# Kernel tuning notes

Hardware: AMD Instinct MI355X
Metric: run time of the kernel (lower is better)

The kernel has to match this reference:

```python
import jax, jax.numpy as jnp
import numpy as np

# GPT-2 decoder (mlm=False path of the Keras GPT module), no past/KV-cache,
# no explicit mask -> causal mask, dropout disabled (training=False).
N_HEAD = 12
NINF = -10000.0  # Attention.ninf
EPS = 1e-6


def layer_norm(x, g, b):
    m = jnp.mean(x, axis=-1, keepdims=True)
    v = jnp.mean(jnp.square(x - m), axis=-1, keepdims=True)
    return (x - m) / jnp.sqrt(v + EPS) * g + b


def gelu(x):
    # 0.5*x*(1+erf(x/sqrt(2))) as in gelu_activating
    return 0.5 * x * (1.0 + jax.lax.erf(x * np.float32(1.0 / np.sqrt(2.0))))


def setup_inputs() -> dict:
    key = jax.random.key(0)
    B, S, D, L, V, CTX = 4, 512, 768, 12, 50257, 1024
    F = 4 * D
    ks = jax.random.split(key, 10)
    init = lambda k, shape: (jax.random.normal(k, shape, jnp.float32) * 0.02)
    return {
        "x": jax.random.randint(ks[0], (B, S), 0, V),
        "emb": init(ks[1], (V, D)),        # wte (tied output projection)
        "posemb": init(ks[2], (CTX, D)),   # wpe
        "ln1_g": jnp.ones((L, D)), "ln1_b": jnp.zeros((L, D)),
        "wqkv": init(ks[3], (L, D, 3 * D)), "bqkv": jnp.zeros((L, 3 * D)),
        "wo": init(ks[4], (L, D, D)), "bo": jnp.zeros((L, D)),
        "ln2_g": jnp.ones((L, D)), "ln2_b": jnp.zeros((L, D)),
        "wfc": init(ks[5], (L, D, F)), "bfc": jnp.zeros((L, F)),
        "wproj": init(ks[6], (L, F, D)), "bproj": jnp.zeros((L, D)),
        "lnf_g": jnp.ones((D,)), "lnf_b": jnp.zeros((D,)),
    }


def reference(x, emb, posemb, ln1_g, ln1_b, wqkv, bqkv, wo, bo,
              ln2_g, ln2_b, wfc, bfc, wproj, bproj, lnf_g, lnf_b):
    B, S = x.shape
    L, D, _ = wqkv.shape
    H = N_HEAD
    hd = D // H
    scale = np.float32(1.0 / np.sqrt(hd))

    # Embedding (mlm=False): token + positional, no layernorm
    h = emb[x] + posemb[:S]  # [B,S,D]

    # causal mask: positions j > i get NINF (m1 = range(q)[:,None] < range(k)-k+q)
    mask = (jnp.arange(S)[:, None] < jnp.arange(S)[None, :]).astype(jnp.float32) * NINF

    for i in range(L):
        # pre-norm attention
        qkv = layer_norm(h, ln1_g[i], ln1_b[i]) @ wqkv[i] + bqkv[i]  # [B,S,3D]
        q, k, v = jnp.split(qkv, 3, axis=-1)
        q = q.reshape(B, S, H, hd).transpose(0, 2, 1, 3)  # [B,H,S,hd]
        k = k.reshape(B, S, H, hd).transpose(0, 2, 1, 3)
        v = v.reshape(B, S, H, hd).transpose(0, 2, 1, 3)
        scores = jnp.einsum('bhqd,bhkd->bhqk', q, k) * scale + mask
        a = jax.nn.softmax(scores, axis=-1)  # [B,H,S,S]
        o = jnp.einsum('bhqk,bhkd->bhqd', a, v)
        o = o.transpose(0, 2, 1, 3).reshape(B, S, D)
        h = h + (o @ wo[i] + bo[i])  # residual
        # pre-norm MLP
        m = layer_norm(h, ln2_g[i], ln2_b[i])
        h = h + (gelu(m @ wfc[i] + bfc[i]) @ wproj[i] + bproj[i])

    hidden = layer_norm(h, lnf_g, lnf_b)          # model/lnorm_f
    logits = hidden @ emb.T                        # tied embedding projection
    probs = jax.nn.softmax(logits, axis=-1)        # softmax=True
    return (probs, hidden)
```

## Files before the change

kernel.cpp:

```cpp
#include <hip/hip_runtime.h>
#include <hip/hip_bf16.h>

typedef __bf16 bf16_t;
typedef bf16_t bf16x8 __attribute__((ext_vector_type(8)));
typedef float  f32x4  __attribute__((ext_vector_type(4)));

__device__ __forceinline__ void gload16(const void* g, void* l) {
    __builtin_amdgcn_global_load_lds(
        (const __attribute__((address_space(1))) unsigned int*)g,
        (__attribute__((address_space(3))) unsigned int*)l, 16, 0, 0);
}

__device__ __forceinline__ void drain_and_barrier() {
    __builtin_amdgcn_sched_barrier(0);
    asm volatile("s_waitcnt vmcnt(0)" ::: "memory");
    __builtin_amdgcn_s_barrier();
    __builtin_amdgcn_sched_barrier(0);
}

__global__ void embed_kernel(const int* __restrict__ x,
                             const float* __restrict__ emb,
                             const float* __restrict__ pos,
                             float* __restrict__ h,
                             int S, int D, int total)
{
    int i = blockIdx.x * blockDim.x + threadIdx.x;
    if (i >= total) return;
    int d  = i % D;
    int bs = i / D;
    int s  = bs % S;
    h[i] = emb[(long long)x[bs] * D + d] + pos[(long long)s * D + d];
}

__global__ void convert_bf16(const float* __restrict__ in, bf16_t* __restrict__ out, int n4)
{
    int i = blockIdx.x * blockDim.x + threadIdx.x;
    for (; i < n4; i += gridDim.x * blockDim.x) {
        float4 v = ((const float4*)in)[i];
        bf16_t* o = out + (size_t)i * 4;
        o[0] = (bf16_t)v.x; o[1] = (bf16_t)v.y; o[2] = (bf16_t)v.z; o[3] = (bf16_t)v.w;
    }
}

__global__ __launch_bounds__(256) void transpose_to_bf16(
    const float* __restrict__ in, bf16_t* __restrict__ out, int K, int N)
{
    const float* ip = in  + (size_t)blockIdx.z * K * N;
    bf16_t*      op = out + (size_t)blockIdx.z * K * N;
    __shared__ float t[32][33];
    const int n0 = blockIdx.x * 32, k0 = blockIdx.y * 32;
    const int tx = threadIdx.x, ty = threadIdx.y;
#pragma unroll
    for (int u = 0; u < 4; ++u)
        t[ty + u * 8][tx] = ip[(size_t)(k0 + ty + u * 8) * N + (n0 + tx)];
    __syncthreads();
#pragma unroll
    for (int u = 0; u < 4; ++u)
        op[(size_t)(n0 + ty + u * 8) * K + (k0 + tx)] = (bf16_t)t[tx][ty + u * 8];
}

__global__ __launch_bounds__(256) void transpose_v(
    const bf16_t* __restrict__ qkv, bf16_t* __restrict__ vT)
{
    constexpr int S = 512, TD = 2304, D = 768, H = 12;
    const int z = blockIdx.y, bb = z / H, hh = z - bb * H;
    const int k0 = blockIdx.x * 64;
    const bf16_t* src = qkv + (size_t)(bb * S + k0) * TD + 2 * D + hh * 64;
    bf16_t* dst = vT + (size_t)z * 64 * S + k0;
    __shared__ bf16_t sm[64][68];
    const int c = threadIdx.x & 63, rq = threadIdx.x >> 6;
#pragma unroll
    for (int u = 0; u < 16; ++u) {
        const int r = u * 4 + rq;
        sm[r][c] = src[(size_t)r * TD + c];
    }
    __syncthreads();
#pragma unroll
    for (int u = 0; u < 16; ++u) {
        const int d = u * 4 + rq;
        dst[(size_t)d * S + c] = sm[c][d];
    }
}

__global__ __launch_bounds__(256) void layernorm_dual(
    const float* __restrict__ X, const float* __restrict__ g,
    const float* __restrict__ b, bf16_t* __restrict__ Yb,
    float* __restrict__ Yf, int D)
{
    const int row = blockIdx.x;
    const float* xr = X + (long long)row * D;
    const int tid = threadIdx.x;

    float vals[3];
    float s = 0.0f;
#pragma unroll
    for (int u = 0; u < 3; ++u) { vals[u] = xr[tid + u * 256]; s += vals[u]; }

    __shared__ float red[256];
    red[tid] = s;
    __syncthreads();
    for (int off = 128; off > 0; off >>= 1) {
        if (tid < off) red[tid] += red[tid + off];
        __syncthreads();
    }
    const float mean = red[0] / (float)D;
    __syncthreads();

    float vs = 0.0f;
#pragma unroll
    for (int u = 0; u < 3; ++u) { float d = vals[u] - mean; vs += d * d; }
    red[tid] = vs;
    __syncthreads();
    for (int off = 128; off > 0; off >>= 1) {
        if (tid < off) red[tid] += red[tid + off];
        __syncthreads();
    }
    const float var  = red[0] / (float)D;
    const float rstd = rsqrtf(var + 1e-6f);

#pragma unroll
    for (int u = 0; u < 3; ++u) {
        const int c = tid + u * 256;
        const float y = (vals[u] - mean) * rstd * g[c] + b[c];
        Yb[(long long)row * D + c] = (bf16_t)y;
        if (Yf) Yf[(long long)row * D + c] = y;
    }
}

__global__ __launch_bounds__(256) void flash_attn(
    const bf16_t* __restrict__ qkv, const bf16_t* __restrict__ vT,
    bf16_t* __restrict__ o)
{
    constexpr int S = 512, TD = 2304, D = 768, H = 12;
    const int qt = blockIdx.x;
    const int z  = blockIdx.y;
    const int bb = z / H, hh = z - bb * H;
    const int tid = threadIdx.x, lane = tid & 63, w = tid >> 6;
    const int fr = lane & 15, g = lane >> 4, sub = g * 8;

    __shared__ bf16_t kS[2][4096];
    __shared__ bf16_t vS[2][4096];
    __shared__ bf16_t pS[4][32 * 72];

    bf16x8 qf[2][2];
    const bf16_t* qbase = qkv + (size_t)(bb * S + qt * 128 + w * 32) * TD + hh * 64;
#pragma unroll
    for (int m = 0; m < 2; ++m)
#pragma unroll
        for (int ks = 0; ks < 2; ++ks) {
            bf16x8 v = *(const bf16x8*)&qbase[(size_t)(m * 16 + fr) * TD + ks * 32 + sub];
#pragma unroll
            for (int j = 0; j < 8; ++j) v[j] = v[j] * (bf16_t)0.125f;
            qf[m][ks] = v;
        }

    f32x4 oacc[2][4];
    float mrun[2][4], lrun[2][4];
#pragma unroll
    for (int m = 0; m < 2; ++m)
#pragma unroll
        for (int r = 0; r < 4; ++r) { mrun[m][r] = -3.0e38f; lrun[m][r] = 0.0f; }
#pragma unroll
    for (int m = 0; m < 2; ++m)
#pragma unroll
        for (int n = 0; n < 4; ++n)
            oacc[m][n] = (f32x4){0.f, 0.f, 0.f, 0.f};

    int qr[2][4];
#pragma unroll
    for (int m = 0; m < 2; ++m)
#pragma unroll
        for (int r = 0; r < 4; ++r)
            qr[m][r] = qt * 128 + w * 32 + m * 16 + g * 4 + r;

    const int srow8  = lane >> 3;
    const int schunk = (lane & 7) ^ (srow8 & 7);

    const bf16_t* kGbase = qkv + (size_t)(bb * S) * TD + D + hh * 64;
    const bf16_t* vGbase = vT + (size_t)z * 64 * S;
    const int nkv = 2 * qt + 2;

#define STAGE_KV(buf, t)                                                        \
    {                                                                           \
        _Pragma("unroll")                                                       \
        for (int it = 0; it < 2; ++it) {                                        \
            const int row = it * 32 + w * 8 + srow8;                            \
            gload16(kGbase + (size_t)((t) * 64 + row) * TD + schunk * 8,        \
                    &kS[buf][it * 2048 + w * 512]);                             \
            gload16(vGbase + (size_t)row * S + (t) * 64 + schunk * 8,           \
                    &vS[buf][it * 2048 + w * 512]);                             \
        }                                                                       \
    }

    STAGE_KV(0, 0);
    drain_and_barrier();

    int cur = 0;
    for (int t = 0; t < nkv; ++t) {
        if (t + 1 < nkv) STAGE_KV(cur ^ 1, t + 1);

        f32x4 sacc[2][4];
#pragma unroll
        for (int m = 0; m < 2; ++m)
#pragma unroll
            for (int n = 0; n < 4; ++n)
                sacc[m][n] = (f32x4){0.f, 0.f, 0.f, 0.f};
#pragma unroll
        for (int ks = 0; ks < 2; ++ks) {
            bf16x8 bK[4];
#pragma unroll
            for (int n = 0; n < 4; ++n) {
                const int rw = n * 16 + fr;
                const int c  = ks * 4 + g;
                bK[n] = *(const bf16x8*)&kS[cur][rw * 64 + ((c ^ (rw & 7)) << 3)];
            }
#pragma unroll
            for (int m = 0; m < 2; ++m)
#pragma unroll
                for (int n = 0; n < 4; ++n)
                    sacc[m][n] = __builtin_amdgcn_mfma_f32_16x16x32_bf16(
                        qf[m][ks], bK[n], sacc[m][n], 0, 0, 0);
        }

        if (t >= 2 * qt) {
#pragma unroll
            for (int m = 0; m < 2; ++m)
#pragma unroll
                for (int n = 0; n < 4; ++n) {
                    const int key = t * 64 + n * 16 + fr;
#pragma unroll
                    for (int r = 0; r < 4; ++r)
                        if (key > qr[m][r]) sacc[m][n][r] = -3.0e38f;
                }
        }

        float sf[2][4], rs[2][4];
#pragma unroll
        for (int m = 0; m < 2; ++m)
#pragma unroll
            for (int r = 0; r < 4; ++r) {
                float v = fmaxf(fmaxf(sacc[m][0][r], sacc[m][1][r]),
                                fmaxf(sacc[m][2][r], sacc[m][3][r]));
#pragma unroll
                for (int off = 1; off < 16; off <<= 1)
                    v = fmaxf(v, __shfl_xor(v, off));
                const float mn = fmaxf(mrun[m][r], v);
                sf[m][r] = __expf(mrun[m][r] - mn);
                mrun[m][r] = mn;
                lrun[m][r] *= sf[m][r];
            }
#pragma unroll
        for (int m = 0; m < 2; ++m)
#pragma unroll
            for (int n = 0; n < 4; ++n)
#pragma unroll
                for (int r = 0; r < 4; ++r)
                    oacc[m][n][r] *= sf[m][r];
#pragma unroll
        for (int m = 0; m < 2; ++m)
#pragma unroll
            for (int r = 0; r < 4; ++r) rs[m][r] = 0.0f;
#pragma unroll
        for (int m = 0; m < 2; ++m)
#pragma unroll
            for (int n = 0; n < 4; ++n)
#pragma unroll
                for (int r = 0; r < 4; ++r) {
                    const float p = __expf(sacc[m][n][r] - mrun[m][r]);
                    sacc[m][n][r] = p;
                    rs[m][r] += p;
                }
#pragma unroll
        for (int m = 0; m < 2; ++m)
#pragma unroll
            for (int r = 0; r < 4; ++r) {
                float v = rs[m][r];
#pragma unroll
                for (int off = 1; off < 16; off <<= 1) v += __shfl_xor(v, off);
                lrun[m][r] += v;
            }

        bf16_t* pw = pS[w];
#pragma unroll
        for (int m = 0; m < 2; ++m)
#pragma unroll
            for (int n = 0; n < 4; ++n)
#pragma unroll
                for (int r = 0; r < 4; ++r)
                    pw[(m * 16 + g * 4 + r) * 72 + n * 16 + fr] = (bf16_t)sacc[m][n][r];

#pragma unroll
        for (int ks = 0; ks < 2; ++ks) {
            bf16x8 pa[2], vb[4];
#pragma unroll
            for (int m = 0; m < 2; ++m)
                pa[m] = *(const bf16x8*)&pw[(m * 16 + fr) * 72 + ks * 32 + sub];
#pragma unroll
            for (int n = 0; n < 4; ++n) {
                const int rw = n * 16 + fr;
                const int c  = ks * 4 + g;
                vb[n] = *(const bf16x8*)&vS[cur][rw * 64 + ((c ^ (rw & 7)) << 3)];
            }
#pragma unroll
            for (int m = 0; m < 2; ++m)
#pragma unroll
                for (int n = 0; n < 4; ++n)
                    oacc[m][n] = __builtin_amdgcn_mfma_f32_16x16x32_bf16(
                        pa[m], vb[n], oacc[m][n], 0, 0, 0);
        }
        drain_and_barrier();
        cur ^= 1;
    }
#undef STAGE_KV

    bf16_t* obase = o + (size_t)(bb * S + qt * 128 + w * 32) * D + hh * 64;
#pragma unroll
    for (int m = 0; m < 2; ++m)
#pragma unroll
        for (int r = 0; r < 4; ++r) {
            const float inv = 1.0f / lrun[m][r];
#pragma unroll
            for (int n = 0; n < 4; ++n)
                obase[(size_t)(m * 16 + g * 4 + r) * D + n * 16 + fr] =
                    (bf16_t)(oacc[m][n][r] * inv);
        }
}

__global__ __launch_bounds__(256) void softmax_vocab(
    const bf16_t* __restrict__ logits, float* __restrict__ probs, int V, int Vp)
{
    const int tid = threadIdx.x;
    const bf16_t* lr = logits + (size_t)blockIdx.x * Vp;
    float* pr = probs + (size_t)blockIdx.x * V;
    const int n8 = V >> 3;

    float m = -3.0e38f, s = 0.0f;
    for (int c8 = tid; c8 < n8; c8 += 256) {
        const bf16x8 v = *(const bf16x8*)(lr + (size_t)c8 * 8);
        float f[8], lm = -3.0e38f;
#pragma unroll
        for (int j = 0; j < 8; ++j) { f[j] = (float)v[j]; lm = fmaxf(lm, f[j]); }
        if (lm > m) { s *= __expf(m - lm); m = lm; }
#pragma unroll
        for (int j = 0; j < 8; ++j) s += __expf(f[j] - m);
    }
    for (int c = n8 * 8 + tid; c < V; c += 256) {
        const float f = (float)lr[c];
        if (f > m) { s *= __expf(m - f); m = f; }
        s += __expf(f - m);
    }

    __shared__ float mS[256], sS[256];
    mS[tid] = m; sS[tid] = s;
    __syncthreads();
    for (int off = 128; off > 0; off >>= 1) {
        if (tid < off) {
            const float m1 = mS[tid], m2 = mS[tid + off];
            const float M_ = fmaxf(m1, m2);
            sS[tid] = sS[tid] * __expf(m1 - M_) + sS[tid + off] * __expf(m2 - M_);
            mS[tid] = M_;
        }
        __syncthreads();
    }
    const float M_  = mS[0];
    const float inv = 1.0f / sS[0];

    for (int c8 = tid; c8 < n8; c8 += 256) {
        const bf16x8 v = *(const bf16x8*)(lr + (size_t)c8 * 8);
#pragma unroll
        for (int j = 0; j < 8; ++j)
            pr[(size_t)c8 * 8 + j] = __expf((float)v[j] - M_) * inv;
    }
    for (int c = n8 * 8 + tid; c < V; c += 256)
        pr[c] = __expf((float)lr[c] - M_) * inv;
}

template<bool ADD, bool GELU_, bool OUTBF, bool DB, bool HALFN>
__device__ __forceinline__ void gemm_body(
    const bf16_t* __restrict__ A, const bf16_t* __restrict__ Bw,
    const float* __restrict__ bias, void* __restrict__ Cv,
    int M, int N, int K, int lda, int ldb, int ldc)
{
    constexpr int BN  = HALFN ? 64 : 128;
    constexpr int BUF = HALFN ? 12288 : 16384;
    __shared__ bf16_t lds[(DB ? 2 : 1) * BUF];

    const int tid  = threadIdx.x;
    const int lane = tid & 63;
    const int w    = tid >> 6;
    const int row0 = blockIdx.x * 128;
    const int col0 = blockIdx.y * BN;

    const int row8 = lane >> 3;
    const int sch  = (lane & 7) ^ row8;
    const int fr   = lane & 15;
    const int g    = lane >> 4;

    const int aRowB = row0 + w * 32;
    const int bRowB = HALFN ? (col0 + w * 16) : (col0 + w * 32);

    constexpr int MR = HALFN ? 2 : 4;
    const int wr = HALFN ? w : (w >> 1);
    const int wc = HALFN ? 0 : (w & 1);

    f32x4 acc[MR][4];
#pragma unroll
    for (int m = 0; m < MR; ++m)
#pragma unroll
        for (int n = 0; n < 4; ++n)
            acc[m][n] = (f32x4){0.f, 0.f, 0.f, 0.f};

    auto STAGE = [&](int buf, int k0) {
        bf16_t* lb = lds + buf * BUF;
#pragma unroll
        for (int it = 0; it < 4; ++it) {
            const int ar = aRowB + it * 8 + row8;
            gload16(A + (size_t)ar * lda + k0 + sch * 8, lb + w * 2048 + it * 512);
        }
#pragma unroll
        for (int it = 0; it < (HALFN ? 2 : 4); ++it) {
            int br = bRowB + it * 8 + row8;
            if (br >= N) br = 0;
            gload16(Bw + (size_t)br * ldb + k0 + sch * 8,
                    lb + 8192 + w * (HALFN ? 1024 : 2048) + it * 512);
        }
    };

    auto COMPUTE = [&](int buf) {
        bf16_t* lb = lds + buf * BUF;
#pragma unroll
        for (int ks = 0; ks < 2; ++ks) {
            bf16x8 af[MR], bfr[4];
            const int cs = ks * 4 + g;
#pragma unroll
            for (int m = 0; m < MR; ++m) {
                const int row = (HALFN ? w * 32 : wr * 64) + m * 16 + fr;
                af[m] = *(const bf16x8*)&lb[row * 64 + ((cs ^ (fr & 7)) << 3)];
            }
#pragma unroll
            for (int n = 0; n < 4; ++n) {
                const int row = (HALFN ? 0 : wc * 64) + n * 16 + fr;
                bfr[n] = *(const bf16x8*)&lb[8192 + row * 64 + ((cs ^ (fr & 7)) << 3)];
            }
#pragma unroll
            for (int m = 0; m < MR; ++m)
#pragma unroll
                for (int n = 0; n < 4; ++n)
                    acc[m][n] = __builtin_amdgcn_mfma_f32_16x16x32_bf16(
                        af[m], bfr[n], acc[m][n], 0, 0, 0);
        }
    };

    const int nt = K >> 6;
    if (DB) {
        STAGE(0, 0);
        drain_and_barrier();
        int cur = 0;
        for (int t = 0; t < nt; ++t) {
            if (t + 1 < nt) STAGE(cur ^ 1, (t + 1) << 6);
            COMPUTE(cur);
            drain_and_barrier();
            cur ^= 1;
        }
    } else {
        for (int t = 0; t < nt; ++t) {
            STAGE(0, t << 6);
            __syncthreads();
            COMPUTE(0);
            __syncthreads();
        }
    }

    const int rBase = row0 + (HALFN ? w * 32 : wr * 64) + g * 4;
    const int cBase = col0 + (HALFN ? 0 : wc * 64) + fr;
    float bv[4];
#pragma unroll
    for (int n = 0; n < 4; ++n) {
        const int c = cBase + n * 16;
        bv[n] = (bias && c < N) ? bias[c] : 0.0f;
    }
#pragma unroll
    for (int m = 0; m < MR; ++m) {
#pragma unroll
        for (int r = 0; r < 4; ++r) {
            const int rr = rBase + m * 16 + r;
#pragma unroll
            for (int n = 0; n < 4; ++n) {
                const int c = cBase + n * 16;
                if (c >= N) continue;
                float v = acc[m][n][r] + bv[n];
                if (GELU_) v = 0.5f * v * (1.0f + erff(v * 0.70710678118654752f));
                if (OUTBF) {
                    ((bf16_t*)Cv)[(size_t)rr * ldc + c] = (bf16_t)v;
                } else {
                    float* Cf = (float*)Cv;
                    const size_t idx = (size_t)rr * ldc + c;
                    if (ADD) v += Cf[idx];
                    Cf[idx] = v;
                }
            }
        }
    }
}

__global__ __launch_bounds__(256) void k_gemm_qkv(
    const bf16_t* A, const bf16_t* B, const float* bias, void* C,
    int M, int N, int K, int lda, int ldb, int ldc)
{ gemm_body<false, false, true, true, false>(A, B, bias, C, M, N, K, lda, ldb, ldc); }

__global__ __launch_bounds__(256) void k_gemm_oproj(
    const bf16_t* A, const bf16_t* B, const float* bias, void* C,
    int M, int N, int K, int lda, int ldb, int ldc)
{ gemm_body<true, false, false, true, true>(A, B, bias, C, M, N, K, lda, ldb, ldc); }

__global__ __launch_bounds__(256) void k_gemm_fc(
    const bf16_t* A, const bf16_t* B, const float* bias, void* C,
    int M, int N, int K, int lda, int ldb, int ldc)
{ gemm_body<false, true, true, true, false>(A, B, bias, C, M, N, K, lda, ldb, ldc); }

__global__ __launch_bounds__(256) void k_gemm_proj(
    const bf16_t* A, const bf16_t* B, const float* bias, void* C,
    int M, int N, int K, int lda, int ldb, int ldc)
{ gemm_body<true, false, false, true, true>(A, B, bias, C, M, N, K, lda, ldb, ldc); }

__global__ __launch_bounds__(256) void k_gemm_head(
    const bf16_t* A, const bf16_t* B, const float* bias, void* C,
    int M, int N, int K, int lda, int ldb, int ldc)
{ gemm_body<false, false, true, false, false>(A, B, bias, C, M, N, K, lda, ldb, ldc); }

extern "C" void kernel_launch(void* const* d_in, const int* in_sizes, int n_in,
                              void* d_out, int out_size, void* d_ws, size_t ws_size,
                              hipStream_t stream)
{
    constexpr int B = 4, S = 512, D = 768, L = 12, V = 50257, H = 12, F = 3072;
    constexpr int M  = B * S;
    constexpr int TD = 3 * D;
    constexpr int BH = B * H;
    constexpr int Vp = 50264;

    const int*   x    = (const int*)  d_in[0];
    const float* emb  = (const float*)d_in[1];
    const float* pos  = (const float*)d_in[2];
    const float* ln1g = (const float*)d_in[3];
    const float* ln1b = (const float*)d_in[4];
    const float* wqkv = (const float*)d_in[5];
    const float* bqkv = (const float*)d_in[6];
    const float* wo   = (const float*)d_in[7];
    const float* bo   = (const float*)d_in[8];
    const float* ln2g = (const float*)d_in[9];
    const float* ln2b = (const float*)d_in[10];
    const float* wfc  = (const float*)d_in[11];
    const float* bfc  = (const float*)d_in[12];
    const float* wpr  = (const float*)d_in[13];
    const float* bpr  = (const float*)d_in[14];
    const float* lnfg = (const float*)d_in[15];
    const float* lnfb = (const float*)d_in[16];

    float* probs  = (float*)d_out;
    float* hidden = probs + (size_t)M * V;

    float*  h      = (float*)d_ws;
    bf16_t* qkv_bf = (bf16_t*)(h + (size_t)M * D);
    bf16_t* vT     = qkv_bf + (size_t)M * TD;
    bf16_t* xn_bf  = vT     + (size_t)BH * 64 * S;
    bf16_t* o_bf   = xn_bf  + (size_t)M * D;
    bf16_t* mid_bf = o_bf   + (size_t)M * D;
    bf16_t* wqkvT  = mid_bf + (size_t)M * F;
    bf16_t* woT    = wqkvT  + (size_t)L * D * TD;
    bf16_t* wfcT   = woT    + (size_t)L * D * D;
    bf16_t* wprT   = wfcT   + (size_t)L * D * F;
    bf16_t* hid_bf = wprT   + (size_t)L * F * D;
    bf16_t* embB   = hid_bf + (size_t)M * D;
    bf16_t* logits = (bf16_t*)d_ws;

    convert_bf16<<<2048, 256, 0, stream>>>(emb, embB, (V * D) / 4);
    transpose_to_bf16<<<dim3(TD / 32, D / 32, L), dim3(32, 8), 0, stream>>>(wqkv, wqkvT, D, TD);
    transpose_to_bf16<<<dim3(D / 32,  D / 32, L), dim3(32, 8), 0, stream>>>(wo,   woT,   D, D);
    transpose_to_bf16<<<dim3(F / 32,  D / 32, L), dim3(32, 8), 0, stream>>>(wfc,  wfcT,  D, F);
    transpose_to_bf16<<<dim3(D / 32,  F / 32, L), dim3(32, 8), 0, stream>>>(wpr,  wprT,  F, D);

    embed_kernel<<<dim3((M * D + 255) / 256), 256, 0, stream>>>(x, emb, pos, h, S, D, M * D);

    for (int i = 0; i < L; ++i) {
        layernorm_dual<<<M, 256, 0, stream>>>(h, ln1g + (size_t)i * D, ln1b + (size_t)i * D,
                                              xn_bf, nullptr, D);

        k_gemm_qkv<<<dim3(M / 128, TD / 128), 256, 0, stream>>>(
            xn_bf, wqkvT + (size_t)i * D * TD, bqkv + (size_t)i * TD, qkv_bf,
            M, TD, D, D, D, TD);

        transpose_v<<<dim3(S / 64, BH), 256, 0, stream>>>(qkv_bf, vT);

        flash_attn<<<dim3(S / 128, BH), 256, 0, stream>>>(qkv_bf, vT, o_bf);

        k_gemm_oproj<<<dim3(M / 128, D / 64), 256, 0, stream>>>(
            o_bf, woT + (size_t)i * D * D, bo + (size_t)i * D, h,
            M, D, D, D, D, D);

        layernorm_dual<<<M, 256, 0, stream>>>(h, ln2g + (size_t)i * D, ln2b + (size_t)i * D,
                                              xn_bf, nullptr, D);

        k_gemm_fc<<<dim3(M / 128, F / 128), 256, 0, stream>>>(
            xn_bf, wfcT + (size_t)i * D * F, bfc + (size_t)i * F, mid_bf,
            M, F, D, D, D, F);

        k_gemm_proj<<<dim3(M / 128, D / 64), 256, 0, stream>>>(
            mid_bf, wprT + (size_t)i * F * D, bpr + (size_t)i * D, h,
            M, D, F, F, F, D);
    }

    layernorm_dual<<<M, 256, 0, stream>>>(h, lnfg, lnfb, hid_bf, hidden, D);

    k_gemm_head<<<dim3(M / 128, (V + 127) / 128), 256, 0, stream>>>(
        hid_bf, embB, nullptr, logits,
        M, V, D, D, D, Vp);

    softmax_vocab<<<M, 256, 0, stream>>>(logits, probs, V, Vp);
}
```

Before: 2.396 ms.

## Add 128x256 LM-head GEMM kernel and use narrow tiles for QKV/FC

```diff
diff --git a/kernel.cpp b/kernel.cpp
--- a/kernel.cpp
+++ b/kernel.cpp
@@ -506,7 +506,7 @@
 __global__ __launch_bounds__(256) void k_gemm_qkv(
     const bf16_t* A, const bf16_t* B, const float* bias, void* C,
     int M, int N, int K, int lda, int ldb, int ldc)
-{ gemm_body<false, false, true, true, false>(A, B, bias, C, M, N, K, lda, ldb, ldc); }
+{ gemm_body<false, false, true, true, true>(A, B, bias, C, M, N, K, lda, ldb, ldc); }
 
 __global__ __launch_bounds__(256) void k_gemm_oproj(
     const bf16_t* A, const bf16_t* B, const float* bias, void* C,
@@ -516,7 +516,7 @@
 __global__ __launch_bounds__(256) void k_gemm_fc(
     const bf16_t* A, const bf16_t* B, const float* bias, void* C,
     int M, int N, int K, int lda, int ldb, int ldc)
-{ gemm_body<false, true, true, true, false>(A, B, bias, C, M, N, K, lda, ldb, ldc); }
+{ gemm_body<false, true, true, true, true>(A, B, bias, C, M, N, K, lda, ldb, ldc); }
 
 __global__ __launch_bounds__(256) void k_gemm_proj(
     const bf16_t* A, const bf16_t* B, const float* bias, void* C,
@@ -524,9 +524,94 @@
 { gemm_body<true, false, false, true, true>(A, B, bias, C, M, N, K, lda, ldb, ldc); }
 
 __global__ __launch_bounds__(256) void k_gemm_head(
-    const bf16_t* A, const bf16_t* B, const float* bias, void* C,
-    int M, int N, int K, int lda, int ldb, int ldc)
-{ gemm_body<false, false, true, false, false>(A, B, bias, C, M, N, K, lda, ldb, ldc); }
+    const bf16_t* __restrict__ A, const bf16_t* __restrict__ Bw,
+    bf16_t* __restrict__ C, int M, int N, int K, int lda, int ldb, int ldc)
+{
+    __shared__ bf16_t lds[24576];
+
+    const int tid  = threadIdx.x;
+    const int lane = tid & 63;
+    const int w    = tid >> 6;
+    const int wr   = w >> 1, wc = w & 1;
+    const int row0 = blockIdx.x * 128;
+    const int col0 = blockIdx.y * 256;
+
+    const int row8 = lane >> 3;
+    const int sch  = (lane & 7) ^ row8;
+    const int fr   = lane & 15;
+    const int g    = lane >> 4;
+
+    const int aRowB = row0 + w * 32;
+    const int bRowB = col0 + w * 64;
+
+    f32x4 acc[4][8];
+#pragma unroll
+    for (int m = 0; m < 4; ++m)
+#pragma unroll
+        for (int n = 0; n < 8; ++n)
+            acc[m][n] = (f32x4){0.f, 0.f, 0.f, 0.f};
+
+    for (int k0 = 0; k0 < K; k0 += 64) {
+#pragma unroll
+        for (int it = 0; it < 4; ++it) {
+            const int ar = aRowB + it * 8 + row8;
+            gload16(A + (size_t)ar * lda + k0 + sch * 8, lds + w * 2048 + it * 512);
+        }
+#pragma unroll
+        for (int it = 0; it < 8; ++it) {
+            int br = bRowB + it * 8 + row8;
+            if (br >= N) br = 0;
+            gload16(Bw + (size_t)br * ldb + k0 + sch * 8,
+                    lds + 8192 + w * 4096 + it * 512);
+        }
+        __syncthreads();
+
+#pragma unroll
+        for (int ks = 0; ks < 2; ++ks) {
+            const int cs = ks * 4 + g;
+            bf16x8 af[4];
+#pragma unroll
+            for (int m = 0; m < 4; ++m) {
+                const int row = wr * 64 + m * 16 + fr;
+                af[m] = *(const bf16x8*)&lds[row * 64 + ((cs ^ (fr & 7)) << 3)];
+            }
+#pragma unroll
+            for (int hf = 0; hf < 2; ++hf) {
+                bf16x8 bfr[4];
+#pragma unroll
+                for (int n = 0; n < 4; ++n) {
+                    const int row = hf * 128 + wc * 64 + n * 16 + fr;
+                    bfr[n] = *(const bf16x8*)&lds[8192 + row * 64 + ((cs ^ (fr & 7)) << 3)];
+                }
+#pragma unroll
+                for (int m = 0; m < 4; ++m)
+#pragma unroll
+                    for (int n = 0; n < 4; ++n)
+                        acc[m][hf * 4 + n] = __builtin_amdgcn_mfma_f32_16x16x32_bf16(
+                            af[m], bfr[n], acc[m][hf * 4 + n], 0, 0, 0);
+            }
+        }
+        __syncthreads();
+    }
+
+    const int rBase = row0 + wr * 64 + g * 4;
+#pragma unroll
+    for (int m = 0; m < 4; ++m) {
+#pragma unroll
+        for (int r = 0; r < 4; ++r) {
+            const int rr = rBase + m * 16 + r;
+#pragma unroll
+            for (int hf = 0; hf < 2; ++hf) {
+#pragma unroll
+                for (int n = 0; n < 4; ++n) {
+                    const int c = col0 + hf * 128 + wc * 64 + n * 16 + fr;
+                    if (c < N)
+                        C[(size_t)rr * ldc + c] = (bf16_t)acc[m][hf * 4 + n][r];
+                }
+            }
+        }
+    }
+}
 
 extern "C" void kernel_launch(void* const* d_in, const int* in_sizes, int n_in,
                               void* d_out, int out_size, void* d_ws, size_t ws_size,
@@ -585,7 +670,7 @@
         layernorm_dual<<<M, 256, 0, stream>>>(h, ln1g + (size_t)i * D, ln1b + (size_t)i * D,
                                               xn_bf, nullptr, D);
 
-        k_gemm_qkv<<<dim3(M / 128, TD / 128), 256, 0, stream>>>(
+        k_gemm_qkv<<<dim3(M / 128, TD / 64), 256, 0, stream>>>(
             xn_bf, wqkvT + (size_t)i * D * TD, bqkv + (size_t)i * TD, qkv_bf,
             M, TD, D, D, D, TD);
 
@@ -600,7 +685,7 @@
         layernorm_dual<<<M, 256, 0, stream>>>(h, ln2g + (size_t)i * D, ln2b + (size_t)i * D,
                                               xn_bf, nullptr, D);
 
-        k_gemm_fc<<<dim3(M / 128, F / 128), 256, 0, stream>>>(
+        k_gemm_fc<<<dim3(M / 128, F / 64), 256, 0, stream>>>(
             xn_bf, wfcT + (size_t)i * D * F, bfc + (size_t)i * F, mid_bf,
             M, F, D, D, D, F);
 
@@ -611,8 +696,8 @@
 
     layernorm_dual<<<M, 256, 0, stream>>>(h, lnfg, lnfb, hid_bf, hidden, D);
 
-    k_gemm_head<<<dim3(M / 128, (V + 127) / 128), 256, 0, stream>>>(
-        hid_bf, embB, nullptr, logits,
+    k_gemm_head<<<dim3(M / 128, (V + 255) / 256), 256, 0, stream>>>(
+        hid_bf, embB, logits,
         M, V, D, D, D, Vp);
 
     softmax_vocab<<<M, 256, 0, stream>>>(logits, probs, V, Vp);
```

New measurement: 2.370 ms. No clear change (-1.1%).
